# Performance work log

Hardware: AMD Instinct MI355X
Metric: run time of the kernel (lower is better)

Reference implementation:

```python
import jax, jax.numpy as jnp
import numpy as np

EPS = 1e-08
DIM = 256


def setup_inputs() -> dict:
    key = jax.random.key(0)
    k1, k2, k3 = jax.random.split(key, 3)
    B, S, D = 4, 4096, DIM
    x = jax.random.normal(k1, (B, S, D), dtype=jnp.float32)
    mask = jnp.ones((B, S), dtype=bool)
    # params of nn.Linear(dim, dim) and log_temp = log(0.1)
    bound = 1.0 / np.sqrt(D)
    W_v = jax.random.uniform(k2, (D, D), minval=-bound, maxval=bound, dtype=jnp.float32)
    b_v = jax.random.uniform(k3, (D,), minval=-bound, maxval=bound, dtype=jnp.float32)
    log_temp = jnp.log(jnp.asarray(0.1, dtype=jnp.float32))
    return {"x": x, "W_v": W_v, "b_v": b_v, "log_temp": log_temp, "mask": mask}


def reference(x, W_v, b_v, log_temp, mask):
    # temperature = exp(log_temp).clamp_min(1e-5)
    temp = jnp.maximum(jnp.exp(log_temp), 1e-5).astype(x.dtype)
    # squared pairwise euclidean distances (cdist^2), clamped to >= 0
    sq = jnp.sum(x * x, axis=-1)  # [B, S]
    d2 = sq[:, :, None] + sq[:, None, :] - 2.0 * jnp.einsum('bsd,btd->bst', x, x)
    d2 = jnp.maximum(d2, 0.0)  # [B, S, S]
    # Cauchy kernel: 1 / (1 + (dist/temp)^2)
    kernel = 1.0 / (1.0 + d2 / (temp * temp))
    valid = (mask[:, None, :] & mask[:, :, None]).astype(kernel.dtype)
    kernel = kernel * valid
    # row-normalize
    attn = kernel / jnp.maximum(jnp.sum(kernel, axis=-1, keepdims=True), EPS)
    v = x @ W_v.T + b_v  # [B, S, D]
    out = jnp.einsum('bst,btd->bsd', attn, v)
    return out
```

## Files before the change

### kernel.cpp

```cpp
#include <hip/hip_runtime.h>
#include <hip/hip_bf16.h>

#define S 4096
#define D 256
#define NB 4

typedef __attribute__((ext_vector_type(8))) __bf16 bf16x8;
typedef __attribute__((ext_vector_type(8))) short s16x8;
typedef __attribute__((ext_vector_type(4))) short s16x4;
typedef __attribute__((ext_vector_type(4))) float f32x4;

#define MFMA(a, b, c) __builtin_amdgcn_mfma_f32_16x16x32_bf16(a, b, c, 0, 0, 0)
#define MFMA8(a, b, c) __builtin_amdgcn_mfma_f32_16x16x32_fp8_fp8(a, b, c, 0, 0, 0)

__device__ __forceinline__ short f2bf(float f) {
    union { float f; unsigned u; } v; v.f = f;
    unsigned r = v.u + 0x7fffu + ((v.u >> 16) & 1u);
    return (short)(r >> 16);
}

__device__ __forceinline__ void g2lds16(const char* g, char* l) {
    __builtin_amdgcn_global_load_lds(
        (const __attribute__((address_space(1))) unsigned int*)g,
        (__attribute__((address_space(3))) unsigned int*)l, 16, 0, 0);
}

__global__ __launch_bounds__(512) void k_vprojx(const float* __restrict__ x,
                                                const float* __restrict__ Wv,
                                                const float* __restrict__ bv,
                                                unsigned char* __restrict__ xb8,
                                                float* __restrict__ sqg,
                                                short* __restrict__ vt) {
    __shared__ short sX[64 * 264];
    __shared__ short sT[256 * 72];

    const int b  = blockIdx.x >> 6;
    const int s0 = (blockIdx.x & 63) * 64;
    const int tid = threadIdx.x;
    const int w = tid >> 6, lane = tid & 63;
    const int col = lane & 15, quad = lane >> 4;

    #pragma unroll
    for (int it = 0; it < 8; it++) {
        int row = it * 8 + w;
        float4 v = *(const float4*)(x + (size_t)(b * S + s0 + row) * D + lane * 4);
        float ss = v.x * v.x + v.y * v.y + v.z * v.z + v.w * v.w;
        #pragma unroll
        for (int off = 32; off; off >>= 1) ss += __shfl_xor(ss, off, 64);
        s16x4 o;
        o.x = f2bf(v.x); o.y = f2bf(v.y); o.z = f2bf(v.z); o.w = f2bf(v.w);
        *(s16x4*)(sX + row * 264 + lane * 4) = o;
        int p8 = __builtin_amdgcn_cvt_pk_fp8_f32(v.x, v.y, 0, false);
        p8 = __builtin_amdgcn_cvt_pk_fp8_f32(v.z, v.w, p8, true);
        *(int*)(xb8 + (size_t)(b * S + s0 + row) * D +
                (((lane >> 2) ^ (row & 7)) << 4) + (lane & 3) * 4) = p8;
        if (lane == 0) sqg[b * S + s0 + row] = ss;
    }

    bf16x8 wf[2][8];
    #pragma unroll
    for (int ni = 0; ni < 2; ni++)
        #pragma unroll
        for (int ks = 0; ks < 8; ks++) {
            const float* p = Wv + (size_t)(w * 32 + ni * 16 + col) * D + ks * 32 + quad * 8;
            float4 f0 = *(const float4*)p;
            float4 f1 = *(const float4*)(p + 4);
            s16x8 o;
            o[0] = f2bf(f0.x); o[1] = f2bf(f0.y); o[2] = f2bf(f0.z); o[3] = f2bf(f0.w);
            o[4] = f2bf(f1.x); o[5] = f2bf(f1.y); o[6] = f2bf(f1.z); o[7] = f2bf(f1.w);
            wf[ni][ks] = *(bf16x8*)&o;
        }
    __syncthreads();

    f32x4 acc[4][2];
    #pragma unroll
    for (int mi = 0; mi < 4; mi++) {
        acc[mi][0] = (f32x4){0.f, 0.f, 0.f, 0.f};
        acc[mi][1] = (f32x4){0.f, 0.f, 0.f, 0.f};
    }
    #pragma unroll
    for (int ks = 0; ks < 8; ks++) {
        bf16x8 a[4];
        #pragma unroll
        for (int mi = 0; mi < 4; mi++)
            a[mi] = *(const bf16x8*)(sX + (mi * 16 + col) * 264 + ks * 32 + quad * 8);
        #pragma unroll
        for (int mi = 0; mi < 4; mi++) {
            acc[mi][0] = MFMA(a[mi], wf[0][ks], acc[mi][0]);
            acc[mi][1] = MFMA(a[mi], wf[1][ks], acc[mi][1]);
        }
    }

    #pragma unroll
    for (int ni = 0; ni < 2; ni++) {
        int d = w * 32 + ni * 16 + col;
        float bvv = bv[d];
        #pragma unroll
        for (int mi = 0; mi < 4; mi++)
            #pragma unroll
            for (int r = 0; r < 4; r++)
                sT[d * 72 + mi * 16 + quad * 4 + r] = f2bf(acc[mi][ni][r] + bvv);
    }
    __syncthreads();
    {
        int d = tid >> 1, half = (tid & 1) * 32;
        short* dst = vt + (size_t)(b * D + d) * S + s0 + half;
        const short* src = sT + d * 72 + half;
        #pragma unroll
        for (int i = 0; i < 4; i++)
            *(s16x8*)(dst + i * 8) = *(const s16x8*)(src + i * 8);
    }
}

template <int TSPLIT>
__global__ __launch_bounds__(256) void k_attn(const unsigned char* __restrict__ xb8,
                                              const short* __restrict__ vt,
                                              const float* __restrict__ sq,
                                              const float* __restrict__ logt,
                                              float* __restrict__ outp,
                                              float* __restrict__ pex,
                                              float* __restrict__ rws) {
    __shared__ char sXt[2][32 * 256];
    __shared__ short sK[2][64 * 36];
    __shared__ float sRow[64];

    const int tid = threadIdx.x;
    const int w = tid >> 6, lane = tid & 63;
    const int col = lane & 15, quad = lane >> 4;
    const int cx = col & 7;

    int b, th, qt;
    if (TSPLIT == 4) {
        b  = (blockIdx.x >> 1) & 3;
        th = (blockIdx.x & 1) | (((blockIdx.x >> 3) & 1) << 1);
        qt = blockIdx.x >> 4;
    } else if (TSPLIT == 2) {
        b  = (blockIdx.x & 7) >> 1;
        th = blockIdx.x & 1;
        qt = blockIdx.x >> 3;
    } else {
        b = blockIdx.x & 3;
        th = 0;
        qt = blockIdx.x >> 2;
    }
    const int q0 = qt * 64;
    const int t_base = th * (S / TSPLIT);
    const int NT = (S / TSPLIT) / 32;

    float temp = fmaxf(__expf(logt[0]), 1e-5f);
    float t2 = temp * temp;

    const unsigned char* xtb = xb8 + (size_t)b * S * D;
    const short* vtb = vt + (size_t)b * D * S;
    const float* sqb = sq + b * S;

    long xq[8];
    {
        const unsigned char* xrow = xtb + (size_t)(q0 + w * 16 + col) * D;
        #pragma unroll
        for (int ks = 0; ks < 8; ks++)
            xq[ks] = *(const long*)(xrow + (((ks * 2 + (quad >> 1)) ^ cx) << 4) + (quad & 1) * 8);
    }
    float sqq[4];
    #pragma unroll
    for (int rr = 0; rr < 4; rr++)
        sqq[rr] = sqb[q0 + w * 16 + quad * 4 + rr];

    f32x4 acc[4][4];
    #pragma unroll
    for (int mi = 0; mi < 4; mi++)
        #pragma unroll
        for (int ni = 0; ni < 4; ni++)
            acc[mi][ni] = (f32x4){0.f, 0.f, 0.f, 0.f};
    float rs[4] = {0.f, 0.f, 0.f, 0.f};

    {
        const char* g = (const char*)(xtb + (size_t)t_base * D);
        #pragma unroll
        for (int p = 0; p < 2; p++) {
            int c = p * 256 + tid;
            g2lds16(g + c * 16, &sXt[0][c * 16]);
        }
    }

    for (int i = 0; i < NT; i++) {
        const int t0 = t_base + i * 32;
        const int cur = i & 1;
        __syncthreads();

        if (i + 1 < NT) {
            const char* g = (const char*)(xtb + (size_t)(t0 + 32) * D);
            #pragma unroll
            for (int p = 0; p < 2; p++) {
                int c = p * 256 + tid;
                g2lds16(g + c * 16, &sXt[cur ^ 1][c * 16]);
            }
        }

        bf16x8 vb[4];
        if (i > 0) {
            const int tp = t0 - 32;
            #pragma unroll
            for (int ni = 0; ni < 4; ni++)
                vb[ni] = *(const bf16x8*)(vtb + (size_t)(w * 64 + ni * 16 + col) * S + tp + quad * 8);
        }
        float sqt0 = sqb[t0 + col], sqt1 = sqb[t0 + 16 + col];

        f32x4 p2v[2];
        p2v[0] = (f32x4){0.f, 0.f, 0.f, 0.f};
        p2v[1] = (f32x4){0.f, 0.f, 0.f, 0.f};
        #pragma unroll
        for (int ks = 0; ks < 8; ks++) {
            int co = (((ks * 2 + (quad >> 1)) ^ cx) << 4) + (quad & 1) * 8;
            long b0 = *(const long*)(&sXt[cur][col * 256 + co]);
            long b1 = *(const long*)(&sXt[cur][(col + 16) * 256 + co]);
            p2v[0] = MFMA8(xq[ks], b0, p2v[0]);
            p2v[1] = MFMA8(xq[ks], b1, p2v[1]);
        }

        #pragma unroll
        for (int t_ = 0; t_ < 2; t_++) {
            float sqt = t_ ? sqt1 : sqt0;
            int tg = t0 + t_ * 16 + col;
            #pragma unroll
            for (int rr = 0; rr < 4; rr++) {
                float d2 = fmaxf(sqq[rr] + sqt - 2.f * p2v[t_][rr], 0.f);
                float kv = t2 * __builtin_amdgcn_rcpf(t2 + d2);
                if (q0 + w * 16 + quad * 4 + rr == tg) kv = 1.f;
                rs[rr] += kv;
                sK[cur][(w * 16 + quad * 4 + rr) * 36 + t_ * 16 + col] = f2bf(kv);
            }
        }

        if (i > 0) {
            #pragma unroll
            for (int mi = 0; mi < 4; mi++) {
                bf16x8 af = *(const bf16x8*)(&sK[cur ^ 1][(mi * 16 + col) * 36 + quad * 8]);
                #pragma unroll
                for (int ni = 0; ni < 4; ni++)
                    acc[mi][ni] = MFMA(af, vb[ni], acc[mi][ni]);
            }
        }
    }

    __syncthreads();
    {
        const int tp = t_base + (NT - 1) * 32;
        const int cur = (NT - 1) & 1;
        bf16x8 vb[4];
        #pragma unroll
        for (int ni = 0; ni < 4; ni++)
            vb[ni] = *(const bf16x8*)(vtb + (size_t)(w * 64 + ni * 16 + col) * S + tp + quad * 8);
        #pragma unroll
        for (int mi = 0; mi < 4; mi++) {
            bf16x8 af = *(const bf16x8*)(&sK[cur][(mi * 16 + col) * 36 + quad * 8]);
            #pragma unroll
            for (int ni = 0; ni < 4; ni++)
                acc[mi][ni] = MFMA(af, vb[ni], acc[mi][ni]);
        }
    }

    #pragma unroll
    for (int rr = 0; rr < 4; rr++) {
        float v = rs[rr];
        v += __shfl_xor(v, 1, 64);
        v += __shfl_xor(v, 2, 64);
        v += __shfl_xor(v, 4, 64);
        v += __shfl_xor(v, 8, 64);
        if (col == 0) sRow[w * 16 + quad * 4 + rr] = v;
    }
    __syncthreads();

    if (TSPLIT == 1) {
        float* ob = outp + (size_t)(b * S + q0) * D;
        #pragma unroll
        for (int mi = 0; mi < 4; mi++)
            #pragma unroll
            for (int rr = 0; rr < 4; rr++) {
                float rinv = __builtin_amdgcn_rcpf(fmaxf(sRow[mi * 16 + quad * 4 + rr], 1e-8f));
                #pragma unroll
                for (int ni = 0; ni < 4; ni++)
                    ob[(size_t)(mi * 16 + quad * 4 + rr) * D + w * 64 + ni * 16 + col] =
                        acc[mi][ni][rr] * rinv;
            }
    } else {
        if (tid < 64) rws[(size_t)th * NB * S + b * S + q0 + tid] = sRow[tid];
        float* ob = (th == 0 ? outp : pex + (size_t)(th - 1) * NB * S * D) + (size_t)(b * S + q0) * D;
        #pragma unroll
        for (int mi = 0; mi < 4; mi++)
            #pragma unroll
            for (int rr = 0; rr < 4; rr++)
                #pragma unroll
                for (int ni = 0; ni < 4; ni++)
                    ob[(size_t)(mi * 16 + quad * 4 + rr) * D + w * 64 + ni * 16 + col] =
                        acc[mi][ni][rr];
    }
}

template <int TSPLIT>
__global__ __launch_bounds__(256) void k_combine(float* __restrict__ outp,
                                                 const float* __restrict__ pex,
                                                 const float* __restrict__ rws) {
    int i4 = blockIdx.x * 256 + threadIdx.x;
    int gs = i4 >> 6;
    float sum = rws[gs];
    #pragma unroll
    for (int p = 1; p < TSPLIT; p++) sum += rws[(size_t)p * NB * S + gs];
    float rinv = __builtin_amdgcn_rcpf(fmaxf(sum, 1e-8f));
    float4 o = ((const float4*)outp)[i4];
    #pragma unroll
    for (int p = 1; p < TSPLIT; p++) {
        float4 e = ((const float4*)(pex + (size_t)(p - 1) * NB * S * D))[i4];
        o.x += e.x; o.y += e.y; o.z += e.z; o.w += e.w;
    }
    o.x *= rinv; o.y *= rinv; o.z *= rinv; o.w *= rinv;
    ((float4*)outp)[i4] = o;
}

extern "C" void kernel_launch(void* const* d_in, const int* in_sizes, int n_in,
                              void* d_out, int out_size, void* d_ws, size_t ws_size,
                              hipStream_t stream) {
    const float* x    = (const float*)d_in[0];
    const float* Wv   = (const float*)d_in[1];
    const float* bv   = (const float*)d_in[2];
    const float* logt = (const float*)d_in[3];
    float* out = (float*)d_out;

    char* ws = (char*)d_ws;
    unsigned char* xb8 = (unsigned char*)ws;
    short* vt  = (short*)(ws + 4194304);
    float* sq  = (float*)(ws + 12582912);
    float* rws = (float*)(ws + 12648448);
    const size_t pex_off = 12910592u;
    const size_t P = (size_t)NB * S * D * 4u;

    k_vprojx<<<NB * (S / 64), 512, 0, stream>>>(x, Wv, bv, xb8, sq, vt);

    const size_t need4 = pex_off + 3u * P;
    const size_t need2 = pex_off + 1u * P;
    if (ws_size >= need4) {
        float* pex = (float*)(ws + pex_off);
        k_attn<4><<<NB * (S / 64) * 4, 256, 0, stream>>>(xb8, vt, sq, logt, out, pex, rws);
        k_combine<4><<<(NB * S * D / 4) / 256, 256, 0, stream>>>(out, pex, rws);
    } else if (ws_size >= need2) {
        float* pex = (float*)(ws + pex_off);
        k_attn<2><<<NB * (S / 64) * 2, 256, 0, stream>>>(xb8, vt, sq, logt, out, pex, rws);
        k_combine<2><<<(NB * S * D / 4) / 256, 256, 0, stream>>>(out, pex, rws);
    } else {
        k_attn<1><<<NB * (S / 64), 256, 0, stream>>>(xb8, vt, sq, logt, out, nullptr, nullptr);
    }
}
```

Before: 191.4 us.

## Split prep kernel, pad fp8 rows instead of swizzle, store fp16 partials

Splits the projection prologue into a prep kernel that converts x to fp8 with row padding (272 bytes) and pre-converts W_v to bf16 once, followed by a separate V-projection kernel. The attention kernel replaces the XOR swizzle with padded LDS rows for simpler addressing. It also writes all split partial outputs as fp16 to a workspace, and the combine kernel sums them in fp32, which halves partial-output traffic. The costs are an extra kernel launch, slightly larger fp8 buffers and loads, and reduced precision in the partial sums.

```diff
diff --git a/kernel.cpp b/kernel.cpp
--- a/kernel.cpp
+++ b/kernel.cpp
@@ -4,11 +4,13 @@
 #define S 4096
 #define D 256
 #define NB 4
+#define XP 272
 
 typedef __attribute__((ext_vector_type(8))) __bf16 bf16x8;
 typedef __attribute__((ext_vector_type(8))) short s16x8;
 typedef __attribute__((ext_vector_type(4))) short s16x4;
 typedef __attribute__((ext_vector_type(4))) float f32x4;
+typedef __attribute__((ext_vector_type(4))) _Float16 h16x4;
 
 #define MFMA(a, b, c) __builtin_amdgcn_mfma_f32_16x16x32_bf16(a, b, c, 0, 0, 0)
 #define MFMA8(a, b, c) __builtin_amdgcn_mfma_f32_16x16x32_fp8_fp8(a, b, c, 0, 0, 0)
@@ -25,12 +27,41 @@
         (__attribute__((address_space(3))) unsigned int*)l, 16, 0, 0);
 }
 
-__global__ __launch_bounds__(512) void k_vprojx(const float* __restrict__ x,
-                                                const float* __restrict__ Wv,
-                                                const float* __restrict__ bv,
-                                                unsigned char* __restrict__ xb8,
-                                                float* __restrict__ sqg,
-                                                short* __restrict__ vt) {
+__global__ __launch_bounds__(512) void k_prep(const float* __restrict__ x,
+                                              const float* __restrict__ Wv,
+                                              unsigned char* __restrict__ xb8,
+                                              short* __restrict__ wb,
+                                              float* __restrict__ sqg) {
+    const int tid = threadIdx.x, w = tid >> 6, lane = tid & 63;
+    if (blockIdx.x < 256) {
+        const int b = blockIdx.x >> 6, s0 = (blockIdx.x & 63) * 64;
+        #pragma unroll
+        for (int it = 0; it < 8; it++) {
+            int gr = b * S + s0 + it * 8 + w;
+            float4 v = ((const float4*)(x + (size_t)gr * D))[lane];
+            float ss = v.x * v.x + v.y * v.y + v.z * v.z + v.w * v.w;
+            #pragma unroll
+            for (int off = 32; off; off >>= 1) ss += __shfl_xor(ss, off, 64);
+            int p8 = __builtin_amdgcn_cvt_pk_fp8_f32(v.x, v.y, 0, false);
+            p8 = __builtin_amdgcn_cvt_pk_fp8_f32(v.z, v.w, p8, true);
+            *(int*)(xb8 + (size_t)gr * XP + lane * 4) = p8;
+            if (lane == 0) sqg[gr] = ss;
+        }
+    } else {
+        int idx = ((blockIdx.x - 256) * 512 + tid) * 8;
+        float4 f0 = *(const float4*)(Wv + idx);
+        float4 f1 = *(const float4*)(Wv + idx + 4);
+        s16x8 o;
+        o[0] = f2bf(f0.x); o[1] = f2bf(f0.y); o[2] = f2bf(f0.z); o[3] = f2bf(f0.w);
+        o[4] = f2bf(f1.x); o[5] = f2bf(f1.y); o[6] = f2bf(f1.z); o[7] = f2bf(f1.w);
+        *(s16x8*)(wb + idx) = o;
+    }
+}
+
+__global__ __launch_bounds__(512) void k_vproj(const float* __restrict__ x,
+                                               const short* __restrict__ wb,
+                                               const float* __restrict__ bv,
+                                               short* __restrict__ vt) {
     __shared__ short sX[64 * 264];
     __shared__ short sT[256 * 72];
 
@@ -40,36 +71,21 @@
     const int w = tid >> 6, lane = tid & 63;
     const int col = lane & 15, quad = lane >> 4;
 
+    bf16x8 wf[2][8];
+    #pragma unroll
+    for (int ni = 0; ni < 2; ni++)
+        #pragma unroll
+        for (int ks = 0; ks < 8; ks++)
+            wf[ni][ks] = *(const bf16x8*)(wb + (size_t)(w * 32 + ni * 16 + col) * D + ks * 32 + quad * 8);
+
     #pragma unroll
     for (int it = 0; it < 8; it++) {
         int row = it * 8 + w;
         float4 v = *(const float4*)(x + (size_t)(b * S + s0 + row) * D + lane * 4);
-        float ss = v.x * v.x + v.y * v.y + v.z * v.z + v.w * v.w;
-        #pragma unroll
-        for (int off = 32; off; off >>= 1) ss += __shfl_xor(ss, off, 64);
         s16x4 o;
         o.x = f2bf(v.x); o.y = f2bf(v.y); o.z = f2bf(v.z); o.w = f2bf(v.w);
         *(s16x4*)(sX + row * 264 + lane * 4) = o;
-        int p8 = __builtin_amdgcn_cvt_pk_fp8_f32(v.x, v.y, 0, false);
-        p8 = __builtin_amdgcn_cvt_pk_fp8_f32(v.z, v.w, p8, true);
-        *(int*)(xb8 + (size_t)(b * S + s0 + row) * D +
-                (((lane >> 2) ^ (row & 7)) << 4) + (lane & 3) * 4) = p8;
-        if (lane == 0) sqg[b * S + s0 + row] = ss;
-    }
-
-    bf16x8 wf[2][8];
-    #pragma unroll
-    for (int ni = 0; ni < 2; ni++)
-        #pragma unroll
-        for (int ks = 0; ks < 8; ks++) {
-            const float* p = Wv + (size_t)(w * 32 + ni * 16 + col) * D + ks * 32 + quad * 8;
-            float4 f0 = *(const float4*)p;
-            float4 f1 = *(const float4*)(p + 4);
-            s16x8 o;
-            o[0] = f2bf(f0.x); o[1] = f2bf(f0.y); o[2] = f2bf(f0.z); o[3] = f2bf(f0.w);
-            o[4] = f2bf(f1.x); o[5] = f2bf(f1.y); o[6] = f2bf(f1.z); o[7] = f2bf(f1.w);
-            wf[ni][ks] = *(bf16x8*)&o;
-        }
+    }
     __syncthreads();
 
     f32x4 acc[4][2];
@@ -118,26 +134,21 @@
                                               const float* __restrict__ sq,
                                               const float* __restrict__ logt,
                                               float* __restrict__ outp,
-                                              float* __restrict__ pex,
+                                              _Float16* __restrict__ pex,
                                               float* __restrict__ rws) {
-    __shared__ char sXt[2][32 * 256];
+    __shared__ char sXt[2][32 * XP];
     __shared__ short sK[2][64 * 36];
     __shared__ float sRow[64];
 
     const int tid = threadIdx.x;
     const int w = tid >> 6, lane = tid & 63;
     const int col = lane & 15, quad = lane >> 4;
-    const int cx = col & 7;
 
     int b, th, qt;
     if (TSPLIT == 4) {
         b  = (blockIdx.x >> 1) & 3;
         th = (blockIdx.x & 1) | (((blockIdx.x >> 3) & 1) << 1);
         qt = blockIdx.x >> 4;
-    } else if (TSPLIT == 2) {
-        b  = (blockIdx.x & 7) >> 1;
-        th = blockIdx.x & 1;
-        qt = blockIdx.x >> 3;
     } else {
         b = blockIdx.x & 3;
         th = 0;
@@ -150,16 +161,16 @@
     float temp = fmaxf(__expf(logt[0]), 1e-5f);
     float t2 = temp * temp;
 
-    const unsigned char* xtb = xb8 + (size_t)b * S * D;
+    const unsigned char* xtb = xb8 + (size_t)b * S * XP;
     const short* vtb = vt + (size_t)b * D * S;
     const float* sqb = sq + b * S;
 
     long xq[8];
     {
-        const unsigned char* xrow = xtb + (size_t)(q0 + w * 16 + col) * D;
+        const unsigned char* xrow = xtb + (size_t)(q0 + w * 16 + col) * XP + quad * 8;
         #pragma unroll
         for (int ks = 0; ks < 8; ks++)
-            xq[ks] = *(const long*)(xrow + (((ks * 2 + (quad >> 1)) ^ cx) << 4) + (quad & 1) * 8);
+            xq[ks] = *(const long*)(xrow + ks * 32);
     }
     float sqq[4];
     #pragma unroll
@@ -175,12 +186,10 @@
     float rs[4] = {0.f, 0.f, 0.f, 0.f};
 
     {
-        const char* g = (const char*)(xtb + (size_t)t_base * D);
-        #pragma unroll
-        for (int p = 0; p < 2; p++) {
-            int c = p * 256 + tid;
-            g2lds16(g + c * 16, &sXt[0][c * 16]);
-        }
+        const char* g = (const char*)(xtb + (size_t)t_base * XP);
+        g2lds16(g + tid * 16, &sXt[0][tid * 16]);
+        g2lds16(g + (tid + 256) * 16, &sXt[0][(tid + 256) * 16]);
+        if (tid < 32) g2lds16(g + (tid + 512) * 16, &sXt[0][(tid + 512) * 16]);
     }
 
     for (int i = 0; i < NT; i++) {
@@ -189,12 +198,11 @@
         __syncthreads();
 
         if (i + 1 < NT) {
-            const char* g = (const char*)(xtb + (size_t)(t0 + 32) * D);
-            #pragma unroll
-            for (int p = 0; p < 2; p++) {
-                int c = p * 256 + tid;
-                g2lds16(g + c * 16, &sXt[cur ^ 1][c * 16]);
-            }
+            const char* g = (const char*)(xtb + (size_t)(t0 + 32) * XP);
+            char* l = sXt[cur ^ 1];
+            g2lds16(g + tid * 16, l + tid * 16);
+            g2lds16(g + (tid + 256) * 16, l + (tid + 256) * 16);
+            if (tid < 32) g2lds16(g + (tid + 512) * 16, l + (tid + 512) * 16);
         }
 
         bf16x8 vb[4];
@@ -209,13 +217,15 @@
         f32x4 p2v[2];
         p2v[0] = (f32x4){0.f, 0.f, 0.f, 0.f};
         p2v[1] = (f32x4){0.f, 0.f, 0.f, 0.f};
-        #pragma unroll
-        for (int ks = 0; ks < 8; ks++) {
-            int co = (((ks * 2 + (quad >> 1)) ^ cx) << 4) + (quad & 1) * 8;
-            long b0 = *(const long*)(&sXt[cur][col * 256 + co]);
-            long b1 = *(const long*)(&sXt[cur][(col + 16) * 256 + co]);
-            p2v[0] = MFMA8(xq[ks], b0, p2v[0]);
-            p2v[1] = MFMA8(xq[ks], b1, p2v[1]);
+        {
+            const char* base = &sXt[cur][col * XP + quad * 8];
+            #pragma unroll
+            for (int ks = 0; ks < 8; ks++) {
+                long b0 = *(const long*)(base + ks * 32);
+                long b1 = *(const long*)(base + 16 * XP + ks * 32);
+                p2v[0] = MFMA8(xq[ks], b0, p2v[0]);
+                p2v[1] = MFMA8(xq[ks], b1, p2v[1]);
+            }
         }
 
         #pragma unroll
@@ -285,7 +295,7 @@
             }
     } else {
         if (tid < 64) rws[(size_t)th * NB * S + b * S + q0 + tid] = sRow[tid];
-        float* ob = (th == 0 ? outp : pex + (size_t)(th - 1) * NB * S * D) + (size_t)(b * S + q0) * D;
+        _Float16* ob = pex + (size_t)th * NB * S * D + (size_t)(b * S + q0) * D;
         #pragma unroll
         for (int mi = 0; mi < 4; mi++)
             #pragma unroll
@@ -293,13 +303,13 @@
                 #pragma unroll
                 for (int ni = 0; ni < 4; ni++)
                     ob[(size_t)(mi * 16 + quad * 4 + rr) * D + w * 64 + ni * 16 + col] =
-                        acc[mi][ni][rr];
+                        (_Float16)acc[mi][ni][rr];
     }
 }
 
 template <int TSPLIT>
 __global__ __launch_bounds__(256) void k_combine(float* __restrict__ outp,
-                                                 const float* __restrict__ pex,
+                                                 const _Float16* __restrict__ pex,
                                                  const float* __restrict__ rws) {
     int i4 = blockIdx.x * 256 + threadIdx.x;
     int gs = i4 >> 6;
@@ -307,11 +317,11 @@
     #pragma unroll
     for (int p = 1; p < TSPLIT; p++) sum += rws[(size_t)p * NB * S + gs];
     float rinv = __builtin_amdgcn_rcpf(fmaxf(sum, 1e-8f));
-    float4 o = ((const float4*)outp)[i4];
-    #pragma unroll
-    for (int p = 1; p < TSPLIT; p++) {
-        float4 e = ((const float4*)(pex + (size_t)(p - 1) * NB * S * D))[i4];
-        o.x += e.x; o.y += e.y; o.z += e.z; o.w += e.w;
+    float4 o = {0.f, 0.f, 0.f, 0.f};
+    #pragma unroll
+    for (int p = 0; p < TSPLIT; p++) {
+        h16x4 e = *(const h16x4*)(pex + (size_t)p * NB * S * D + (size_t)i4 * 4);
+        o.x += (float)e[0]; o.y += (float)e[1]; o.z += (float)e[2]; o.w += (float)e[3];
     }
     o.x *= rinv; o.y *= rinv; o.z *= rinv; o.w *= rinv;
     ((float4*)outp)[i4] = o;
@@ -328,24 +338,19 @@
 
     char* ws = (char*)d_ws;
     unsigned char* xb8 = (unsigned char*)ws;
-    short* vt  = (short*)(ws + 4194304);
-    float* sq  = (float*)(ws + 12582912);
-    float* rws = (float*)(ws + 12648448);
-    const size_t pex_off = 12910592u;
-    const size_t P = (size_t)NB * S * D * 4u;
-
-    k_vprojx<<<NB * (S / 64), 512, 0, stream>>>(x, Wv, bv, xb8, sq, vt);
-
-    const size_t need4 = pex_off + 3u * P;
-    const size_t need2 = pex_off + 1u * P;
-    if (ws_size >= need4) {
-        float* pex = (float*)(ws + pex_off);
+    short* wb  = (short*)(ws + 4456448);
+    short* vt  = (short*)(ws + 4587520);
+    float* sq  = (float*)(ws + 12976128);
+    float* rws = (float*)(ws + 13041664);
+    _Float16* pex = (_Float16*)(ws + 13303808);
+    const size_t PH = (size_t)NB * S * D * 2u;
+
+    k_prep<<<272, 512, 0, stream>>>(x, Wv, xb8, wb, sq);
+    k_vproj<<<NB * (S / 64), 512, 0, stream>>>(x, wb, bv, vt);
+
+    if (ws_size >= 13303808u + 4u * PH) {
         k_attn<4><<<NB * (S / 64) * 4, 256, 0, stream>>>(xb8, vt, sq, logt, out, pex, rws);
         k_combine<4><<<(NB * S * D / 4) / 256, 256, 0, stream>>>(out, pex, rws);
-    } else if (ws_size >= need2) {
-        float* pex = (float*)(ws + pex_off);
-        k_attn<2><<<NB * (S / 64) * 2, 256, 0, stream>>>(xb8, vt, sq, logt, out, pex, rws);
-        k_combine<2><<<(NB * S * D / 4) / 256, 256, 0, stream>>>(out, pex, rws);
     } else {
         k_attn<1><<<NB * (S / 64), 256, 0, stream>>>(xb8, vt, sq, logt, out, nullptr, nullptr);
     }
```

Result: slower. 206.7 us (+8.0%).
